# Kernel tuning notes

Hardware: AMD Instinct MI355X
Metric: run time of the kernel (lower is better)

The kernel has to match this reference:

```python
import jax, jax.numpy as jnp
import numpy as np
from jax.scipy.ndimage import map_coordinates

N, H, W = 64, 1024, 1024

def setup_inputs() -> dict:
    key = jax.random.key(0)
    k1, k2, k3 = jax.random.split(key, 3)
    inputs = jax.random.normal(k1, (1, N, H, W, 1), dtype=jnp.float32)
    flux = jax.random.normal(k2, (N, 1, 1, 1), dtype=jnp.float32) * 0.05  # tf.random_normal_initializer stddev
    noise = jnp.zeros((N, 1, 1, 1), dtype=jnp.float32)
    dydx = jax.random.normal(k3, (N, 2), dtype=jnp.float32)  # sub-pixel shifts
    return {"inputs": inputs, "flux": flux, "noise": noise, "dydx": dydx}

def reference(inputs, flux, noise, dydx):
    # inputs: [1, N, H, W, 1]; per-frame bilinear shift (scipy order=1, mode='mirror'),
    # then elementwise flux scale + noise bias.
    x = inputs[0, ..., 0]  # [N, H, W]
    yy = jnp.arange(H, dtype=jnp.float32)[:, None]  # [H,1]
    xx = jnp.arange(W, dtype=jnp.float32)[None, :]  # [1,W]

    def shift_one(img, s):
        # scipy.ndimage.shift: output[i,j] = input[i - dy, j - dx], bilinear, mirror boundary
        cy = jnp.broadcast_to(yy - s[0], (H, W))
        cx = jnp.broadcast_to(xx - s[1], (H, W))
        return map_coordinates(img, [cy, cx], order=1, mode='mirror')

    shifted = jax.vmap(shift_one)(x, dydx)  # [N, H, W]
    shifted = shifted.reshape(inputs.shape)  # [1, N, H, W, 1]
    return shifted * flux + noise
```

## Files before the change

### kernel.cpp

```cpp
#include <hip/hip_runtime.h>

#define NFRAMES 64
#define HH 1024
#define WW 1024

typedef float f32x4 __attribute__((ext_vector_type(4)));

__device__ __forceinline__ int mirror_fix(int idx, int s, int m) {
    int t = (idx + s) % m;
    if (t < 0) t += m;
    t -= s;
    return t < 0 ? -t : t;
}

template<int O>
__device__ __forceinline__ void compute_patch(const f32x4 (&L)[5][2],
                                              float fy, float gy,
                                              float fx, float gx,
                                              float fl, float bi,
                                              f32x4 (&res)[4]) {
    float w[5][5];
    #pragma unroll
    for (int r = 0; r < 5; ++r) {
        #pragma unroll
        for (int c = 0; c < 5; ++c) {
            const int idx = O + c;
            w[r][c] = (idx < 4) ? L[r][0][idx & 3] : L[r][1][idx & 3];
        }
    }
    #pragma unroll
    for (int r = 0; r < 4; ++r) {
        float t[5];
        #pragma unroll
        for (int c = 0; c < 5; ++c) t[c] = gy * w[r][c] + fy * w[r + 1][c];
        res[r][0] = (gx * t[0] + fx * t[1]) * fl + bi;
        res[r][1] = (gx * t[1] + fx * t[2]) * fl + bi;
        res[r][2] = (gx * t[2] + fx * t[3]) * fl + bi;
        res[r][3] = (gx * t[3] + fx * t[4]) * fl + bi;
    }
}

__global__ __launch_bounds__(256) void
flux_shift_kernel(const float* __restrict__ in,
                  const float* __restrict__ flux,
                  const float* __restrict__ noise,
                  const float* __restrict__ dydx,
                  float* __restrict__ out) {
    const int bid = blockIdx.x;
    const int swz = ((bid & 7) << 11) | (bid >> 3);
    const int band = swz & 255;
    const int n    = swz >> 8;
    const int y0   = band << 2;
    const int x    = threadIdx.x << 2;

    const float dy = dydx[2 * n];
    const float dx = dydx[2 * n + 1];
    const float fl = flux[n];
    const float bi = noise[n];

    const float nky = floorf(-dy);
    const float nkx = floorf(-dx);
    const float fy = -dy - nky;
    const float fx = -dx - nkx;
    const int ky = (int)nky;
    const int kx = (int)nkx;
    const float gy = 1.0f - fy;
    const float gx = 1.0f - fx;

    const int ry = y0 + ky;
    const int o  = kx & 3;
    const int A  = x + kx - o;

    const float* __restrict__ base = in + (size_t)n * (HH * WW);
    float* __restrict__ ob = out + (size_t)n * (HH * WW) + (size_t)y0 * WW + x;

    if (ry >= 0 && ry + 4 <= HH - 1 && A >= 0 && A <= WW - 8) {
        const float* __restrict__ p = base + (size_t)ry * WW + A;
        f32x4 L[5][2];
        #pragma unroll
        for (int r = 0; r < 5; ++r) {
            L[r][0] = *reinterpret_cast<const f32x4*>(p + (size_t)r * WW);
            L[r][1] = *reinterpret_cast<const f32x4*>(p + (size_t)r * WW + 4);
        }
        f32x4 res[4];
        switch (o) {
            case 0:  compute_patch<0>(L, fy, gy, fx, gx, fl, bi, res); break;
            case 1:  compute_patch<1>(L, fy, gy, fx, gx, fl, bi, res); break;
            case 2:  compute_patch<2>(L, fy, gy, fx, gx, fl, bi, res); break;
            default: compute_patch<3>(L, fy, gy, fx, gx, fl, bi, res); break;
        }
        #pragma unroll
        for (int r = 0; r < 4; ++r)
            __builtin_nontemporal_store(res[r],
                reinterpret_cast<f32x4*>(ob + (size_t)r * WW));
    } else {
        const int sh = HH - 1, mh = 2 * sh;
        const int sw = WW - 1, mw = 2 * sw;
        const int cx0 = x + kx;
        #pragma unroll
        for (int r = 0; r < 4; ++r) {
            const int iy0 = mirror_fix(y0 + r + ky,     sh, mh);
            const int iy1 = mirror_fix(y0 + r + ky + 1, sh, mh);
            const float* __restrict__ r0 = base + (size_t)iy0 * WW;
            const float* __restrict__ r1 = base + (size_t)iy1 * WW;
            f32x4 res;
            #pragma unroll
            for (int j = 0; j < 4; ++j) {
                const int c0 = mirror_fix(cx0 + j,     sw, mw);
                const int c1 = mirror_fix(cx0 + j + 1, sw, mw);
                const float t0 = gy * r0[c0] + fy * r1[c0];
                const float t1 = gy * r0[c1] + fy * r1[c1];
                res[j] = (gx * t0 + fx * t1) * fl + bi;
            }
            __builtin_nontemporal_store(res,
                reinterpret_cast<f32x4*>(ob + (size_t)r * WW));
        }
    }
}

extern "C" void kernel_launch(void* const* d_in, const int* in_sizes, int n_in,
                              void* d_out, int out_size, void* d_ws, size_t ws_size,
                              hipStream_t stream) {
    const float* in    = (const float*)d_in[0];
    const float* flux  = (const float*)d_in[1];
    const float* noise = (const float*)d_in[2];
    const float* dydx  = (const float*)d_in[3];
    float* out = (float*)d_out;

    const int grid  = NFRAMES * (HH / 4);
    const int block = 256;

    flux_shift_kernel<<<grid, block, 0, stream>>>(in, flux, noise, dydx, out);
}
```

Measured before the change: 451.9 us.

## Process 64-row chunks per block with rolling row registers and border fixup

Each block now covers a 64-row strip of one frame and keeps a rolling window of four rows in registers. This removes the re-read of the halo row that each 4-row tile needed and prefetches the next row while computing the current one. Column borders are handled by clamping the load address and then overwriting the edge columns in a separate scalar pass after a barrier, so the main path no longer branches on the boundary. The grid shrinks from 16384 to 1024 blocks, which reduces parallelism and latency hiding on a 256-CU device, and the nontemporal stores are replaced by plain stores.

```diff
diff --git a/kernel.cpp b/kernel.cpp
--- a/kernel.cpp
+++ b/kernel.cpp
@@ -3,41 +3,83 @@
 #define NFRAMES 64
 #define HH 1024
 #define WW 1024
+#define CHUNK 64
+#define SH (HH - 1)
+#define SW (WW - 1)
 
 typedef float f32x4 __attribute__((ext_vector_type(4)));
 
-__device__ __forceinline__ int mirror_fix(int idx, int s, int m) {
-    int t = (idx + s) % m;
-    if (t < 0) t += m;
-    t -= s;
-    return t < 0 ? -t : t;
+__device__ __forceinline__ int reflect(int i, int s) {
+    if (i < 0) i = -i;
+    if (i > s) i = 2 * s - i;
+    return i;
 }
 
 template<int O>
-__device__ __forceinline__ void compute_patch(const f32x4 (&L)[5][2],
-                                              float fy, float gy,
-                                              float fx, float gx,
-                                              float fl, float bi,
-                                              f32x4 (&res)[4]) {
-    float w[5][5];
-    #pragma unroll
-    for (int r = 0; r < 5; ++r) {
-        #pragma unroll
-        for (int c = 0; c < 5; ++c) {
-            const int idx = O + c;
-            w[r][c] = (idx < 4) ? L[r][0][idx & 3] : L[r][1][idx & 3];
-        }
+__device__ __forceinline__ void extract5(const f32x4 a, const f32x4 b, float (&w)[5]) {
+#pragma unroll
+    for (int c = 0; c < 5; ++c) {
+        const int idx = O + c;
+        w[c] = (idx < 4) ? a[idx] : b[idx - 4];
     }
-    #pragma unroll
-    for (int r = 0; r < 4; ++r) {
-        float t[5];
-        #pragma unroll
-        for (int c = 0; c < 5; ++c) t[c] = gy * w[r][c] + fy * w[r + 1][c];
-        res[r][0] = (gx * t[0] + fx * t[1]) * fl + bi;
-        res[r][1] = (gx * t[1] + fx * t[2]) * fl + bi;
-        res[r][2] = (gx * t[2] + fx * t[3]) * fl + bi;
-        res[r][3] = (gx * t[3] + fx * t[4]) * fl + bi;
+}
+
+template<int O>
+__device__ __forceinline__ void run_chunk(const float* __restrict__ fin,
+                                          float* __restrict__ fout,
+                                          int y0, int ky, int A,
+                                          float fy, float gy,
+                                          float Gx, float Fx, float bi) {
+    const int x  = threadIdx.x << 2;
+    const int rb = y0 + ky;
+
+    f32x4 r0a, r0b, r1a, r1b, r2a, r2b, r3a, r3b;
+    {
+        const float* p0 = fin + (size_t)reflect(rb + 0, SH) * WW;
+        const float* p1 = fin + (size_t)reflect(rb + 1, SH) * WW;
+        const float* p2 = fin + (size_t)reflect(rb + 2, SH) * WW;
+        const float* p3 = fin + (size_t)reflect(rb + 3, SH) * WW;
+        r0a = *(const f32x4*)(p0 + A); r0b = *(const f32x4*)(p0 + A + 4);
+        r1a = *(const f32x4*)(p1 + A); r1b = *(const f32x4*)(p1 + A + 4);
+        r2a = *(const f32x4*)(p2 + A); r2b = *(const f32x4*)(p2 + A + 4);
+        r3a = *(const f32x4*)(p3 + A); r3b = *(const f32x4*)(p3 + A + 4);
     }
+
+#define SUBITER(J, LOA, LOB, HIA, HIB, PF)                                     \
+    {                                                                          \
+        float wl[5], wh[5];                                                    \
+        extract5<O>(LOA, LOB, wl);                                             \
+        extract5<O>(HIA, HIB, wh);                                             \
+        if (PF) {   \
+            const float* pp = fin + (size_t)reflect(rb + (J) + 4, SH) * WW;    \
+            LOA = *(const f32x4*)(pp + A);                                     \
+            LOB = *(const f32x4*)(pp + A + 4);                                 \
+        }                                                                      \
+        const float t0 = gy * wl[0] + fy * wh[0];                              \
+        const float t1 = gy * wl[1] + fy * wh[1];                              \
+        const float t2 = gy * wl[2] + fy * wh[2];                              \
+        const float t3 = gy * wl[3] + fy * wh[3];                              \
+        const float t4 = gy * wl[4] + fy * wh[4];                              \
+        f32x4 ov;                                                              \
+        ov[0] = fmaf(Gx, t0, fmaf(Fx, t1, bi));                                \
+        ov[1] = fmaf(Gx, t1, fmaf(Fx, t2, bi));                                \
+        ov[2] = fmaf(Gx, t2, fmaf(Fx, t3, bi));                                \
+        ov[3] = fmaf(Gx, t3, fmaf(Fx, t4, bi));                                \
+        *(f32x4*)(fout + (size_t)(y0 + (J)) * WW + x) = ov;                    \
+    }
+
+    int j = 0;
+    for (int m = 0; m < CHUNK / 4 - 1; ++m, j += 4) {
+        SUBITER(j + 0, r0a, r0b, r1a, r1b, true)
+        SUBITER(j + 1, r1a, r1b, r2a, r2b, true)
+        SUBITER(j + 2, r2a, r2b, r3a, r3b, true)
+        SUBITER(j + 3, r3a, r3b, r0a, r0b, true)
+    }
+    SUBITER(j + 0, r0a, r0b, r1a, r1b, true)
+    SUBITER(j + 1, r1a, r1b, r2a, r2b, false)
+    SUBITER(j + 2, r2a, r2b, r3a, r3b, false)
+    SUBITER(j + 3, r3a, r3b, r0a, r0b, false)
+#undef SUBITER
 }
 
 __global__ __launch_bounds__(256) void
@@ -46,12 +88,9 @@
                   const float* __restrict__ noise,
                   const float* __restrict__ dydx,
                   float* __restrict__ out) {
-    const int bid = blockIdx.x;
-    const int swz = ((bid & 7) << 11) | (bid >> 3);
-    const int band = swz & 255;
-    const int n    = swz >> 8;
-    const int y0   = band << 2;
-    const int x    = threadIdx.x << 2;
+    const int chunk = blockIdx.x & (HH / CHUNK - 1);
+    const int n     = blockIdx.x >> 4;
+    const int y0    = chunk * CHUNK;
 
     const float dy = dydx[2 * n];
     const float dx = dydx[2 * n + 1];
@@ -66,55 +105,43 @@
     const int kx = (int)nkx;
     const float gy = 1.0f - fy;
     const float gx = 1.0f - fx;
+    const float Gx = gx * fl, Fx = fx * fl;
 
-    const int ry = y0 + ky;
-    const int o  = kx & 3;
-    const int A  = x + kx - o;
+    const int x = threadIdx.x << 2;
+    const int o = kx & 3;
+    int A = x + kx - o;
+    A = A < 0 ? 0 : (A > WW - 8 ? WW - 8 : A);
 
-    const float* __restrict__ base = in + (size_t)n * (HH * WW);
-    float* __restrict__ ob = out + (size_t)n * (HH * WW) + (size_t)y0 * WW + x;
+    const float* __restrict__ fin  = in  + (size_t)n * (HH * WW);
+    float* __restrict__       fout = out + (size_t)n * (HH * WW);
 
-    if (ry >= 0 && ry + 4 <= HH - 1 && A >= 0 && A <= WW - 8) {
-        const float* __restrict__ p = base + (size_t)ry * WW + A;
-        f32x4 L[5][2];
+    switch (o) {
+        case 0:  run_chunk<0>(fin, fout, y0, ky, A, fy, gy, Gx, Fx, bi); break;
+        case 1:  run_chunk<1>(fin, fout, y0, ky, A, fy, gy, Gx, Fx, bi); break;
+        case 2:  run_chunk<2>(fin, fout, y0, ky, A, fy, gy, Gx, Fx, bi); break;
+        default: run_chunk<3>(fin, fout, y0, ky, A, fy, gy, Gx, Fx, bi); break;
+    }
+
+    __syncthreads();
+
+    for (int f = threadIdx.x; f < CHUNK * 6; f += 256) {
+        const int rr = f / 6;
+        const int qe = f - rr * 6;
+        const int q  = qe < 3 ? qe : 250 + qe;
+        const int yy = y0 + rr;
+        const float* __restrict__ p0 = fin + (size_t)reflect(yy + ky,     SH) * WW;
+        const float* __restrict__ p1 = fin + (size_t)reflect(yy + ky + 1, SH) * WW;
+        const int cx0 = (q << 2) + kx;
+        f32x4 ov;
         #pragma unroll
-        for (int r = 0; r < 5; ++r) {
-            L[r][0] = *reinterpret_cast<const f32x4*>(p + (size_t)r * WW);
-            L[r][1] = *reinterpret_cast<const f32x4*>(p + (size_t)r * WW + 4);
+        for (int jj = 0; jj < 4; ++jj) {
+            const int c0 = reflect(cx0 + jj,     SW);
+            const int c1 = reflect(cx0 + jj + 1, SW);
+            const float t0 = gy * p0[c0] + fy * p1[c0];
+            const float t1 = gy * p0[c1] + fy * p1[c1];
+            ov[jj] = fmaf(Gx, t0, fmaf(Fx, t1, bi));
         }
-        f32x4 res[4];
-        switch (o) {
-            case 0:  compute_patch<0>(L, fy, gy, fx, gx, fl, bi, res); break;
-            case 1:  compute_patch<1>(L, fy, gy, fx, gx, fl, bi, res); break;
-            case 2:  compute_patch<2>(L, fy, gy, fx, gx, fl, bi, res); break;
-            default: compute_patch<3>(L, fy, gy, fx, gx, fl, bi, res); break;
-        }
-        #pragma unroll
-        for (int r = 0; r < 4; ++r)
-            __builtin_nontemporal_store(res[r],
-                reinterpret_cast<f32x4*>(ob + (size_t)r * WW));
-    } else {
-        const int sh = HH - 1, mh = 2 * sh;
-        const int sw = WW - 1, mw = 2 * sw;
-        const int cx0 = x + kx;
-        #pragma unroll
-        for (int r = 0; r < 4; ++r) {
-            const int iy0 = mirror_fix(y0 + r + ky,     sh, mh);
-            const int iy1 = mirror_fix(y0 + r + ky + 1, sh, mh);
-            const float* __restrict__ r0 = base + (size_t)iy0 * WW;
-            const float* __restrict__ r1 = base + (size_t)iy1 * WW;
-            f32x4 res;
-            #pragma unroll
-            for (int j = 0; j < 4; ++j) {
-                const int c0 = mirror_fix(cx0 + j,     sw, mw);
-                const int c1 = mirror_fix(cx0 + j + 1, sw, mw);
-                const float t0 = gy * r0[c0] + fy * r1[c0];
-                const float t1 = gy * r0[c1] + fy * r1[c1];
-                res[j] = (gx * t0 + fx * t1) * fl + bi;
-            }
-            __builtin_nontemporal_store(res,
-                reinterpret_cast<f32x4*>(ob + (size_t)r * WW));
-        }
+        *(f32x4*)(fout + (size_t)yy * WW + (q << 2)) = ov;
     }
 }
 
@@ -127,7 +154,7 @@
     const float* dydx  = (const float*)d_in[3];
     float* out = (float*)d_out;
 
-    const int grid  = NFRAMES * (HH / 4);
+    const int grid  = NFRAMES * (HH / CHUNK);
     const int block = 256;
 
     flux_shift_kernel<<<grid, block, 0, stream>>>(in, flux, noise, dydx, out);
```

Measured after the change: 449.6 us. No clear change (-0.5%).
